# Optimization experiments

Hardware: AMD Instinct MI355X
Metric: run time of the kernel (lower is better)

## Reference

```python
import jax, jax.numpy as jnp
import numpy as np

EPS_L2 = 1e-6   # featureL2Norm epsilon
EPS_MM = 1e-5   # MutualMatching epsilon
K_POOL = 2      # relocalization_k_size


def feature_l2norm(f):
    # torch: f / sqrt(sum(f^2, dim=1) + eps)
    norm = jnp.sqrt(jnp.sum(f * f, axis=1, keepdims=True) + EPS_L2)
    return f / norm


def mutual_matching(c):
    # c: [b, 1, f1, f2, f3, f4]
    b_max = jnp.max(c, axis=(2, 3), keepdims=True)  # max over source positions
    a_max = jnp.max(c, axis=(4, 5), keepdims=True)  # max over target positions
    return c * (c / (a_max + EPS_MM)) * (c / (b_max + EPS_MM))


def maxpool4d_max(c, k):
    # c: [b, 1, H, W, H2, W2] -> strided 4D max pool (max over all k^4 offsets)
    b = c.shape[0]
    H, W, H2, W2 = c.shape[2:]
    x = c[:, 0].reshape(b, H // k, k, W // k, k, H2 // k, k, W2 // k, k)
    x = x.transpose(0, 1, 3, 5, 7, 2, 4, 6, 8)
    x = x.reshape(b, H // k, W // k, H2 // k, W2 // k, k ** 4)
    return jnp.max(x, axis=-1)[:, None]  # [b,1,H/k,W/k,H2/k,W2/k]


def conv4d(x, w, b):
    # x: [N, Cin, d1, d2, d3, d4], w: [Cout, Cin, 3,3,3,3], SAME padding (pre-pad 1)
    y = jax.lax.conv_general_dilated(x, w, window_strides=(1, 1, 1, 1), padding='SAME')
    return y + b.reshape(1, -1, 1, 1, 1, 1)


def setup_inputs() -> dict:
    key = jax.random.key(0)
    ks = jax.random.split(key, 8)
    B, C, H, W = 8, 1024, 48, 48
    return {
        'feature_A': jax.random.normal(ks[0], (B, C, H, W), dtype=jnp.float32),
        'feature_B': jax.random.normal(ks[1], (B, C, H, W), dtype=jnp.float32),
        'w1': jax.random.normal(ks[2], (10, 1, 3, 3, 3, 3), dtype=jnp.float32) * 0.05,
        'b1': jnp.zeros((10,), dtype=jnp.float32),
        'w2': jax.random.normal(ks[3], (10, 10, 3, 3, 3, 3), dtype=jnp.float32) * 0.05,
        'b2': jnp.zeros((10,), dtype=jnp.float32),
        'w3': jax.random.normal(ks[4], (1, 10, 3, 3, 3, 3), dtype=jnp.float32) * 0.05,
        'b3': jnp.zeros((1,), dtype=jnp.float32),
    }


def reference(feature_A, feature_B, w1, b1, w2, b2, w3, b3):
    # 1) L2-normalize features over channels
    fa = feature_l2norm(feature_A)
    fb = feature_l2norm(feature_B)
    b, c, h, w = fa.shape
    # 2) 4D correlation: [b, hA*wA, hB*wB]
    corr = jnp.einsum('bcp,bcq->bpq', fa.reshape(b, c, h * w), fb.reshape(b, c, h * w))
    corr = corr.reshape(b, 1, h, w, h, w)
    # ReLU + featureL2Norm over singleton channel dim => x / sqrt(x^2 + eps)
    corr = jax.nn.relu(corr)
    corr = corr / jnp.sqrt(corr * corr + EPS_L2)
    # 3) strided 4D max pool (relocalization)
    corr = maxpool4d_max(corr, K_POOL)
    # 4) mutual matching
    corr = mutual_matching(corr)
    x = jax.nn.relu(conv4d(corr, w1, b1))
    x = jax.nn.relu(conv4d(x, w2, b2))
    x = jax.nn.relu(conv4d(x, w3, b3))
    # 6) mutual matching again
    return mutual_matching(x)
```

## Files before the change

### kernel.cpp

```cpp
#include <hip/hip_runtime.h>
#include <hip/hip_bf16.h>
#include <math.h>

#define C_   1024
#define P_   2304
#define S4   331776

typedef __attribute__((ext_vector_type(8))) short short8;
typedef __attribute__((ext_vector_type(4))) float f32x4;
typedef __attribute__((ext_vector_type(4))) unsigned int u32x4;

__device__ inline unsigned short f2bf(float v) {
  unsigned u = __builtin_bit_cast(unsigned, v);
  u += 0x7fffu + ((u >> 16) & 1u);
  return (unsigned short)(u >> 16);
}
__device__ inline float bf2f(unsigned short h) {
  unsigned u = ((unsigned)h) << 16;
  return __builtin_bit_cast(float, u);
}

__device__ inline void async16(const void* g, void* l) {
  __builtin_amdgcn_global_load_lds(
      (const __attribute__((address_space(1))) unsigned int*)g,
      (__attribute__((address_space(3))) unsigned int*)l, 16, 0, 0);
}

__global__ __launch_bounds__(256) void k_prep(
    const float* __restrict__ fA, const float* __restrict__ fB,
    unsigned short* __restrict__ TAhi, unsigned short* __restrict__ TAlo,
    unsigned short* __restrict__ TBhi, unsigned short* __restrict__ TBlo,
    float* __restrict__ part) {
  __shared__ float ld[64 * 65];
  __shared__ float pslds[512];
  const int c0 = blockIdx.x * 64, p0 = blockIdx.y * 64;
  const int fb = blockIdx.z, f = fb >> 3, b = fb & 7;
  const float* src = (f ? fB : fA) + (size_t)b * C_ * P_;
  unsigned short* Thi = (f ? TBhi : TAhi) + (size_t)b * P_ * C_;
  unsigned short* Tlo = (f ? TBlo : TAlo) + (size_t)b * P_ * C_;
  const int t = threadIdx.x;
#pragma unroll
  for (int e = 0; e < 4; ++e) {
    int cid = t + e * 256;
    int r = cid >> 4, ch = cid & 15;
    float4 v = *(const float4*)&src[(size_t)(c0 + r) * P_ + p0 + ch * 4];
    ld[r * 65 + ch * 4 + 0] = v.x;
    ld[r * 65 + ch * 4 + 1] = v.y;
    ld[r * 65 + ch * 4 + 2] = v.z;
    ld[r * 65 + ch * 4 + 3] = v.w;
  }
  __syncthreads();
#pragma unroll
  for (int e = 0; e < 2; ++e) {
    int ocid = t + e * 256;
    int pl = ocid >> 3, c8 = ocid & 7;
    unsigned short hi[8], lo[8];
    float sq = 0.f;
#pragma unroll
    for (int s = 0; s < 8; ++s) {
      float v = ld[(c8 * 8 + s) * 65 + pl];
      unsigned short h = f2bf(v);
      float rem = v - bf2f(h);
      hi[s] = h; lo[s] = f2bf(rem);
      sq = fmaf(v, v, sq);
    }
    size_t go = (size_t)(p0 + pl) * C_ + c0 + c8 * 8;
    *(uint4*)&Thi[go] = *(uint4*)hi;
    *(uint4*)&Tlo[go] = *(uint4*)lo;
    pslds[ocid] = sq;
  }
  __syncthreads();
  if (t < 64) {
    float s = 0.f;
#pragma unroll
    for (int c8 = 0; c8 < 8; ++c8) s += pslds[t * 8 + c8];
    part[((size_t)fb * 16 + blockIdx.x) * P_ + p0 + t] = s;
  }
}

__global__ void k_invnorm(const float* __restrict__ part, float* __restrict__ inv) {
  int p = blockIdx.x * 256 + threadIdx.x;
  int fb = blockIdx.y;
  float s = 1e-6f;
  for (int ct = 0; ct < 16; ++ct) s += part[((size_t)fb * 16 + ct) * P_ + p];
  inv[(size_t)fb * P_ + p] = 1.0f / sqrtf(s);
}

__global__ __launch_bounds__(256, 3) void k_corr_mfma(
    const unsigned short* __restrict__ TAhi_, const unsigned short* __restrict__ TAlo_,
    const unsigned short* __restrict__ TBhi_, const unsigned short* __restrict__ TBlo_,
    const float* __restrict__ invn, float* __restrict__ pooled) {
  __shared__ __align__(16) char lds_raw[36864];
  float* epi = (float*)lds_raw;

  const int b = blockIdx.y;
  const size_t tb = (size_t)b * P_ * C_;
  const unsigned short* TAhi = TAhi_ + tb;
  const unsigned short* TAlo = TAlo_ + tb;
  const unsigned short* TBhi = TBhi_ + tb;
  const unsigned short* TBlo = TBlo_ + tb;
  float* out = pooled + (size_t)b * S4;

  const int g = blockIdx.x;
  const int xcd = g & 7, idx = g >> 3;
  const int ti = (xcd & 1) * 6 + idx % 6;
  const int tj = (xcd >> 1) * 6 + idx / 6;
  const int p0 = ti * 192, q0 = tj * 96;
  const int t = threadIdx.x;
  const int lane = t & 63, w = t >> 6;
  const int wr = w >> 1, wc = w & 1;
  const int m15 = lane & 15, q4 = lane >> 4;
  const int laneoff = (q4 ^ ((m15 >> 1) & 3)) * 16;

  f32x4 acc[6][3];
#pragma unroll
  for (int a = 0; a < 6; ++a)
#pragma unroll
    for (int c = 0; c < 3; ++c) acc[a][c] = (f32x4){0.f, 0.f, 0.f, 0.f};

  const unsigned short* gld[9];
  int ldsb[9];
#pragma unroll
  for (int e = 0; e < 9; ++e) {
    int chunk = (w * 9 + e) * 64 + lane;
    int row = chunk >> 2, cpos = chunk & 3;
    int cglob = cpos ^ ((row >> 1) & 3);
    const unsigned short* bp; int roff;
    if (row < 192)      { bp = TAhi; roff = p0 + row; }
    else if (row < 384) { bp = TAlo; roff = p0 + row - 192; }
    else if (row < 480) { bp = TBhi; roff = q0 + row - 384; }
    else                { bp = TBlo; roff = q0 + row - 480; }
    gld[e] = bp + (size_t)roff * C_ + cglob * 8;
    ldsb[e] = (w * 9 + e) * 1024;
  }

  auto STAGE = [&](int kt) {
#pragma unroll
    for (int e = 0; e < 9; ++e)
      async16(gld[e] + kt, lds_raw + ldsb[e]);
  };

  for (int kt = 0; kt < C_; kt += 32) {
    __syncthreads();
    STAGE(kt);
    asm volatile("s_waitcnt vmcnt(0)" ::: "memory");
    __syncthreads();

    const char* buf = lds_raw;
    short8 bh[3], bl[3];
#pragma unroll
    for (int c = 0; c < 3; ++c) {
      int rB = (384 + wc * 48 + c * 16 + m15) * 64;
      bh[c] = *(const short8*)(buf + rB + laneoff);
      bl[c] = *(const short8*)(buf + rB + 6144 + laneoff);
    }
#pragma unroll
    for (int a = 0; a < 6; ++a) {
      int rA = (wr * 96 + a * 16 + m15) * 64;
      short8 ah = *(const short8*)(buf + rA + laneoff);
      short8 al = *(const short8*)(buf + rA + 12288 + laneoff);
#pragma unroll
      for (int c = 0; c < 3; ++c)
        acc[a][c] = __builtin_amdgcn_mfma_f32_16x16x32_bf16(ah, bh[c], acc[a][c], 0, 0, 0);
#pragma unroll
      for (int c = 0; c < 3; ++c)
        acc[a][c] = __builtin_amdgcn_mfma_f32_16x16x32_bf16(ah, bl[c], acc[a][c], 0, 0, 0);
#pragma unroll
      for (int c = 0; c < 3; ++c)
        acc[a][c] = __builtin_amdgcn_mfma_f32_16x16x32_bf16(al, bh[c], acc[a][c], 0, 0, 0);
    }
  }
  __syncthreads();

  const float* invA = invn + (size_t)b * P_;
  const float* invB = invn + (size_t)(8 + b) * P_;
  float ibv[3];
#pragma unroll
  for (int c = 0; c < 3; ++c) ibv[c] = invB[q0 + wc * 48 + c * 16 + m15];
#pragma unroll
  for (int a = 0; a < 6; ++a) {
    float4 ia = *(const float4*)&invA[p0 + wr * 96 + a * 16 + q4 * 4];
    int h_local = wr * 2 + (a >= 3 ? 1 : 0);
    int wbase = (a % 3) * 8 + q4 * 2;
#pragma unroll
    for (int c = 0; c < 3; ++c) {
      float v0 = acc[a][c][0] * ia.x * ibv[c];
      float v1 = acc[a][c][1] * ia.y * ibv[c];
      float v2 = acc[a][c][2] * ia.z * ibv[c];
      float v3 = acc[a][c][3] * ia.w * ibv[c];
      float m0 = fmaxf(v0, v1), m1 = fmaxf(v2, v3);
      m0 = fmaxf(m0, __shfl_xor(m0, 1, 64));
      m1 = fmaxf(m1, __shfl_xor(m1, 1, 64));
      if (!(m15 & 1)) {
        int ql2 = wc * 24 + c * 8 + (m15 >> 1);
        epi[(h_local * 24 + wbase + 0) * 50 + ql2] = m0;
        epi[(h_local * 24 + wbase + 1) * 50 + ql2] = m1;
      }
    }
  }
  __syncthreads();

  for (int ix = t; ix < 1152; ix += 256) {
    int orow = ix / 24, ocol = ix % 24;
    int dlt = orow / 24, wp = orow % 24;
    const float* r0 = &epi[((dlt * 2 + 0) * 24 + wp) * 50];
    const float* r1 = &epi[((dlt * 2 + 1) * 24 + wp) * 50];
    float m = fmaxf(fmaxf(r0[ocol], r0[24 + ocol]),
                    fmaxf(r1[ocol], r1[24 + ocol]));
    float r = fmaxf(m, 0.f);
    float v = r / sqrtf(r * r + 1e-6f);
    out[(size_t)(ti * 48 + orow) * 576 + tj * 24 + ocol] = v;
  }
}

__global__ void k_rowmax(const float* __restrict__ x, float* __restrict__ amax) {
  int row = blockIdx.x;
  const float* r = x + (size_t)row * 576;
  float m = -1e30f;
  for (int e = threadIdx.x; e < 576; e += 64) m = fmaxf(m, r[e]);
  for (int off = 32; off > 0; off >>= 1) m = fmaxf(m, __shfl_down(m, off, 64));
  if (threadIdx.x == 0) amax[row] = m;
}

__global__ void k_colmax(const float* __restrict__ x, float* __restrict__ bmax) {
  __shared__ float pl[4][64];
  int b = blockIdx.x, klc = blockIdx.y * 64;
  int t = threadIdx.x;
  int kl = klc + (t & 63), seg = t >> 6;
  const float* xb = x + (size_t)b * S4;
  float m = -1e30f;
  for (int ij = seg * 144; ij < (seg + 1) * 144; ++ij)
    m = fmaxf(m, xb[(size_t)ij * 576 + kl]);
  pl[seg][t & 63] = m;
  __syncthreads();
  if (t < 64) {
    float r = fmaxf(fmaxf(pl[0][t], pl[1][t]), fmaxf(pl[2][t], pl[3][t]));
    bmax[b * 576 + klc + t] = r;
  }
}

__global__ void k_mm_apply(const float* __restrict__ x,
                           const float* __restrict__ amax,
                           const float* __restrict__ bmax,
                           float* __restrict__ y) {
  int i = blockIdx.x * 256 + threadIdx.x;
  int b = i / S4, r = i % S4;
  int ij = r / 576, kl = r % 576;
  float c = x[i];
  y[i] = c * (c / (amax[b * 576 + ij] + 1e-5f)) * (c / (bmax[b * 576 + kl] + 1e-5f));
}

__global__ __launch_bounds__(192, 4) void k_conv1_pack(
    const float* __restrict__ x, const float* __restrict__ w,
    const float* __restrict__ bias, unsigned int* __restrict__ C1p) {
  __shared__ float tile[9 * 702];
  const float* xb = x + (size_t)S4 * blockIdx.y;
  unsigned int* yb = C1p + ((size_t)blockIdx.y * 576 + blockIdx.x) * 6912;
  const int ij = blockIdx.x;
  const int i = ij / 24, j = ij % 24;
  const int t = threadIdx.x;
  const int k = t >> 3;
  const int l0 = (t & 7) * 3;

  if (t < 152) yb[6760 + t] = 0u;
  if (t < 100) {
    int kk, ll;
    if (t < 26)      { kk = 0;          ll = t; }
    else if (t < 52) { kk = 25;         ll = t - 26; }
    else if (t < 76) { kk = t - 52 + 1; ll = 0; }
    else             { kk = t - 76 + 1; ll = 25; }
    unsigned int* p = yb + (kk * 26 + ll) * 10;
#pragma unroll
    for (int q = 0; q < 10; ++q) p[q] = 0u;
  }

  int soff[4]; bool eok[4], klok[4]; int eidx[4];
#pragma unroll
  for (int q = 0; q < 4; ++q) {
    int e = t + q * 192;
    eidx[q] = e; eok[q] = (e < 702);
    int row = e / 27, col = e % 27;
    klok[q] = (row >= 1 && row < 25 && col >= 1 && col < 25);
    soff[q] = (row - 1) * 24 + (col - 1);
  }

  float acc[10][3];
#pragma unroll
  for (int co = 0; co < 10; ++co)
#pragma unroll
    for (int oo = 0; oo < 3; ++oo) acc[co][oo] = 0.f;

#pragma unroll
  for (int pln = 0; pln < 9; ++pln) {
    int ii = i + pln / 3 - 1, jj = j + pln % 3 - 1;
    const bool slab_ok = (ii >= 0 && ii < 24 && jj >= 0 && jj < 24);
    const float* src = xb + (size_t)(ii * 24 + jj) * 576;
#pragma unroll
    for (int q = 0; q < 4; ++q) {
      if (eok[q]) {
        float v = 0.f;
        if (slab_ok && klok[q]) v = src[soff[q]];
        tile[pln * 702 + eidx[q]] = v;
      }
    }
  }
  __syncthreads();
#pragma unroll
  for (int pln = 0; pln < 9; ++pln) {
    const float* base = &tile[pln * 702 + k * 27 + l0];
#pragma unroll
    for (int dk = 0; dk < 3; ++dk) {
      float c0 = base[dk * 27 + 0], c1 = base[dk * 27 + 1],
            c2 = base[dk * 27 + 2], c3 = base[dk * 27 + 3],
            c4 = base[dk * 27 + 4];
#pragma unroll
      for (int co = 0; co < 10; ++co) {
        const float* wr = w + (size_t)co * 81 + pln * 9 + dk * 3;
        float w0 = wr[0], w1 = wr[1], w2v = wr[2];
        acc[co][0] = fmaf(w0, c0, acc[co][0]);
        acc[co][0] = fmaf(w1, c1, acc[co][0]);
        acc[co][0] = fmaf(w2v, c2, acc[co][0]);
        acc[co][1] = fmaf(w0, c1, acc[co][1]);
        acc[co][1] = fmaf(w1, c2, acc[co][1]);
        acc[co][1] = fmaf(w2v, c3, acc[co][1]);
        acc[co][2] = fmaf(w0, c2, acc[co][2]);
        acc[co][2] = fmaf(w1, c3, acc[co][2]);
        acc[co][2] = fmaf(w2v, c4, acc[co][2]);
      }
    }
  }
#pragma unroll
  for (int oo = 0; oo < 3; ++oo) {
    unsigned int* baseo = yb + ((k + 1) * 26 + (l0 + oo + 1)) * 10;
#pragma unroll
    for (int co = 0; co < 10; ++co) {
      float v = fmaxf(acc[co][oo] + bias[co], 0.f);
      unsigned short hi = f2bf(v);
      unsigned short lo = f2bf(v - bf2f(hi));
      baseo[co] = ((unsigned)hi << 16) | (unsigned)lo;
    }
  }
}

__global__ void k_packw2(const float* __restrict__ w2,
                         unsigned short* __restrict__ P1,
                         unsigned short* __restrict__ P2) {
  int idx = blockIdx.x * 256 + threadIdx.x;
  if (idx >= 30720) return;
  int tap = idx >> 10;
  int h   = (idx >> 9) & 1;
  int n   = (idx >> 5) & 15;
  int kp  = idx & 31;
  int k   = h * 16 + (kp >> 1);
  float v = 0.f;
  if (tap < 27 && n < 10 && k < 30) {
    int ci = k % 10, dl = k / 10;
    v = w2[(size_t)(n * 10 + ci) * 81 + tap * 3 + dl];
  }
  unsigned short hi = f2bf(v);
  unsigned short lo = f2bf(v - bf2f(hi));
  P1[idx] = hi;
  P2[idx] = (kp & 1) ? lo : (unsigned short)0;
}

__global__ void k_packw3(const float* __restrict__ w3,
                         unsigned short* __restrict__ Bh,
                         unsigned short* __restrict__ Bl) {
  int idx = blockIdx.x * 256 + threadIdx.x;
  if (idx >= 4608) return;
  int s = idx >> 9;
  int n = (idx >> 5) & 15;
  int kap = idx & 31;
  float v = 0.f;
  if (n < 3 && kap < 30) {
    int ci = kap % 10, dl = kap / 10;
    v = w3[(size_t)ci * 81 + s * 9 + n * 3 + dl];
  }
  unsigned short hi = f2bf(v);
  unsigned short lo = f2bf(v - bf2f(hi));
  Bh[idx] = hi; Bl[idx] = lo;
}

__global__ __launch_bounds__(256, 2) void k_conv2_mfma(
    const unsigned int* __restrict__ C1p,
    const unsigned short* __restrict__ Wp1, const unsigned short* __restrict__ Wp2,
    const float* __restrict__ bias, unsigned int* __restrict__ C2p) {
  __shared__ __align__(16) unsigned int lds[2 * 7168];
  const int b = blockIdx.y, ij = blockIdx.x;
  const int i = ij / 24, j = ij % 24;
  const int t = threadIdx.x, lane = t & 63, w = t >> 6;
  const int m15 = lane & 15, q4 = lane >> 4;

  unsigned int* yb = C2p + ((size_t)b * 576 + ij) * 6912;
  if (t < 152) yb[6760 + t] = 0u;
  if (t < 100) {
    int kk, ll;
    if (t < 26)      { kk = 0;          ll = t; }
    else if (t < 52) { kk = 25;         ll = t - 26; }
    else if (t < 76) { kk = t - 52 + 1; ll = 0; }
    else             { kk = t - 76 + 1; ll = 25; }
    unsigned int* p = yb + (kk * 26 + ll) * 10;
#pragma unroll
    for (int q = 0; q < 10; ++q) p[q] = 0u;
  }

  int rowb[9];
#pragma unroll
  for (int mi = 0; mi < 9; ++mi) {
    int kl = (w * 9 + mi) * 16 + m15;
    int kk = kl / 24, ll = kl % 24;
    rowb[mi] = ((kk + 1) * 26 + ll) * 10;
  }

  const unsigned int* sptr[9]; int tb[9];
#pragma unroll
  for (int s = 0; s < 9; ++s) {
    int di = s / 3 - 1, dj = s % 3 - 1;
    int ii = i + di, jj = j + dj;
    bool v = ((unsigned)ii < 24u) && ((unsigned)jj < 24u);
    sptr[s] = C1p + ((size_t)b * 576 + (size_t)(v ? (ii * 24 + jj) : ij)) * 6912;
    tb[s] = v ? s * 3 : 27;
  }

  auto STAGE = [&](const unsigned int* sp, int par) {
#pragma unroll
    for (int r = 0; r < 7; ++r) {
      const int g = w * 7 + r;
      const unsigned int* gp = sp + (g < 27 ? g * 256 : 0) + lane * 4;
      async16(gp, (char*)lds + par * 28672 + g * 1024);
    }
  };

  f32x4 acc[9];
#pragma unroll
  for (int mi = 0; mi < 9; ++mi) acc[mi] = (f32x4){0.f, 0.f, 0.f, 0.f};

  STAGE(sptr[0], 0);

#pragma unroll
  for (int s = 0; s < 9; ++s) {
    const int par = s & 1;
    short8 p1[3][2], p2[3][2];
#pragma unroll
    for (int dk = 0; dk < 3; ++dk)
#pragma unroll
      for (int h = 0; h < 2; ++h) {
        size_t o = (size_t)(((tb[s] + dk) * 2 + h) * 16 + m15) * 32 + (size_t)q4 * 8;
        p1[dk][h] = *(const short8*)(Wp1 + o);
        p2[dk][h] = *(const short8*)(Wp2 + o);
      }
    if (s < 8) {
      STAGE(sptr[s + 1], par ^ 1);
      asm volatile("s_waitcnt vmcnt(7)" ::: "memory");
    } else {
      asm volatile("s_waitcnt vmcnt(0)" ::: "memory");
    }
    __builtin_amdgcn_s_barrier();
    __builtin_amdgcn_sched_barrier(0);

    const unsigned int* buf = lds + par * 7168;
#pragma unroll
    for (int dk = 0; dk < 3; ++dk) {
#pragma unroll
      for (int mi = 0; mi < 9; ++mi) {
        const char* base = (const char*)(buf + (rowb[mi] + (dk - 1) * 260)) + q4 * 16;
        uint2 a00 = *(const uint2*)(base);
        uint2 a01 = *(const uint2*)(base + 8);
        uint2 a10 = *(const uint2*)(base + 64);
        uint2 a11 = *(const uint2*)(base + 72);
        short8 a0 = __builtin_bit_cast(short8, (u32x4){a00.x, a00.y, a01.x, a01.y});
        short8 a1 = __builtin_bit_cast(short8, (u32x4){a10.x, a10.y, a11.x, a11.y});
        acc[mi] = __builtin_amdgcn_mfma_f32_16x16x32_bf16(a0, p1[dk][0], acc[mi], 0, 0, 0);
        acc[mi] = __builtin_amdgcn_mfma_f32_16x16x32_bf16(a0, p2[dk][0], acc[mi], 0, 0, 0);
        acc[mi] = __builtin_amdgcn_mfma_f32_16x16x32_bf16(a1, p1[dk][1], acc[mi], 0, 0, 0);
        acc[mi] = __builtin_amdgcn_mfma_f32_16x16x32_bf16(a1, p2[dk][1], acc[mi], 0, 0, 0);
      }
    }
    __builtin_amdgcn_sched_barrier(0);
    __builtin_amdgcn_s_barrier();
  }

  if (m15 < 10) {
    const float bv = bias[m15];
#pragma unroll
    for (int mi = 0; mi < 9; ++mi) {
#pragma unroll
      for (int reg = 0; reg < 4; ++reg) {
        int kl = (w * 9 + mi) * 16 + q4 * 4 + reg;
        int kk = kl / 24 + 1, ll = kl % 24 + 1;
        float v = fmaxf(acc[mi][reg] + bv, 0.f);
        unsigned short hi = f2bf(v);
        unsigned short lo = f2bf(v - bf2f(hi));
        yb[(kk * 26 + ll) * 10 + m15] = ((unsigned)hi << 16) | (unsigned)lo;
      }
    }
  }
}

__global__ __launch_bounds__(256, 2) void k_conv3_mfma(
    const unsigned int* __restrict__ C2p,
    const unsigned short* __restrict__ Bh, const unsigned short* __restrict__ Bl,
    const float* __restrict__ bias, float* __restrict__ C3) {
  __shared__ __align__(16) unsigned int lds[2 * 7168];
  const int b = blockIdx.y, ij = blockIdx.x;
  const int i = ij / 24, j = ij % 24;
  const int t = threadIdx.x, lane = t & 63, w = t >> 6;
  const int m15 = lane & 15, q4 = lane >> 4;

  int rowb[10];
#pragma unroll
  for (int mi = 0; mi < 10; ++mi) {
    int m = (w * 10 + mi) * 16 + m15;
    int kp = m / 24, l = m % 24;
    rowb[mi] = (m < 624) ? (kp * 26 + l) * 10 : 0;
  }

  bool sval[9];
  const unsigned int* sptr[9];
#pragma unroll
  for (int s = 0; s < 9; ++s) {
    int di = s / 3 - 1, dj = s % 3 - 1;
    int ii = i + di, jj = j + dj;
    bool v = ((unsigned)ii < 24u) && ((unsigned)jj < 24u);
    sval[s] = v;
    sptr[s] = C2p + ((size_t)b * 576 + (size_t)(v ? (ii * 24 + jj) : ij)) * 6912;
  }

  short8 BHk[9], BLk[9];
#pragma unroll
  for (int s = 0; s < 9; ++s) {
    size_t o = (size_t)(s * 16 + m15) * 32 + (size_t)q4 * 8;
    BHk[s] = *(const short8*)(Bh + o);
    BLk[s] = *(const short8*)(Bl + o);
  }

  auto STAGE = [&](const unsigned int* sp, int par) {
#pragma unroll
    for (int r = 0; r < 7; ++r) {
      const int g = w * 7 + r;
      const unsigned int* gp = sp + (g < 27 ? g * 256 : 0) + lane * 4;
      async16(gp, (char*)lds + par * 28672 + g * 1024);
    }
  };

  f32x4 acc[10];
#pragma unroll
  for (int mi = 0; mi < 10; ++mi) acc[mi] = (f32x4){0.f, 0.f, 0.f, 0.f};

  STAGE(sptr[0], 0);

#pragma unroll
  for (int s = 0; s < 9; ++s) {
    const int par = s & 1;
    if (s < 8) {
      STAGE(sptr[s + 1], par ^ 1);
      asm volatile("s_waitcnt vmcnt(7)" ::: "memory");
    } else {
      asm volatile("s_waitcnt vmcnt(0)" ::: "memory");
    }
    __builtin_amdgcn_s_barrier();
    __builtin_amdgcn_sched_barrier(0);
    if (sval[s]) {
      const unsigned int* buf = lds + par * 7168;
#pragma unroll
      for (int mi = 0; mi < 10; ++mi) {
        const uint2* p = (const uint2*)(buf + rowb[mi] + q4 * 8);
        uint2 d0 = p[0], d1 = p[1], d2 = p[2], d3 = p[3];
        u32x4 hd, lv;
        hd.x = __builtin_amdgcn_perm(d0.y, d0.x, 0x07060302u);
        hd.y = __builtin_amdgcn_perm(d1.y, d1.x, 0x07060302u);
        hd.z = __builtin_amdgcn_perm(d2.y, d2.x, 0x07060302u);
        hd.w = __builtin_amdgcn_perm(d3.y, d3.x, 0x07060302u);
        lv.x = __builtin_amdgcn_perm(d0.y, d0.x, 0x05040100u);
        lv.y = __builtin_amdgcn_perm(d1.y, d1.x, 0x05040100u);
        lv.z = __builtin_amdgcn_perm(d2.y, d2.x, 0x05040100u);
        lv.w = __builtin_amdgcn_perm(d3.y, d3.x, 0x05040100u);
        short8 ah = __builtin_bit_cast(short8, hd);
        short8 al = __builtin_bit_cast(short8, lv);
        acc[mi] = __builtin_amdgcn_mfma_f32_16x16x32_bf16(ah, BHk[s], acc[mi], 0, 0, 0);
        acc[mi] = __builtin_amdgcn_mfma_f32_16x16x32_bf16(ah, BLk[s], acc[mi], 0, 0, 0);
        acc[mi] = __builtin_amdgcn_mfma_f32_16x16x32_bf16(al, BHk[s], acc[mi], 0, 0, 0);
      }
    }
    __builtin_amdgcn_sched_barrier(0);
    __builtin_amdgcn_s_barrier();
  }

  float* u = (float*)lds;
  if (m15 < 3) {
#pragma unroll
    for (int mi = 0; mi < 10; ++mi)
#pragma unroll
      for (int reg = 0; reg < 4; ++reg) {
        int m = (w * 10 + mi) * 16 + q4 * 4 + reg;
        u[m * 4 + m15] = acc[mi][reg];
      }
  }
  __syncthreads();
  const float bv = bias[0];
  float* outp = C3 + (size_t)b * S4 + (size_t)ij * 576;
  for (int idx = t; idx < 576; idx += 256) {
    int k = idx / 24, l = idx % 24;
    float sum = u[((k + 0) * 24 + l) * 4 + 0]
              + u[((k + 1) * 24 + l) * 4 + 1]
              + u[((k + 2) * 24 + l) * 4 + 2];
    outp[idx] = fmaxf(sum + bv, 0.f);
  }
}

extern "C" void kernel_launch(void* const* d_in, const int* in_sizes, int n_in,
                              void* d_out, int out_size, void* d_ws, size_t ws_size,
                              hipStream_t stream) {
  const float* fA = (const float*)d_in[0];
  const float* fB = (const float*)d_in[1];
  const float* w1 = (const float*)d_in[2];
  const float* b1 = (const float*)d_in[3];
  const float* w2 = (const float*)d_in[4];
  const float* b2 = (const float*)d_in[5];
  const float* w3 = (const float*)d_in[6];
  const float* b3 = (const float*)d_in[7];
  float* out = (float*)d_out;
  float* ws = (float*)d_ws;
  (void)in_sizes; (void)n_in; (void)out_size; (void)ws_size;

  unsigned int* C1p  = (unsigned int*)ws;
  unsigned int* C2p  = (unsigned int*)(ws + 31850496);
  unsigned short* TAhi = (unsigned short*)ws;
  unsigned short* TAlo = TAhi + (size_t)8 * P_ * C_;
  unsigned short* TBhi = TAlo + (size_t)8 * P_ * C_;
  unsigned short* TBlo = TBhi + (size_t)8 * P_ * C_;
  float* pooled = ws + 37748736;
  float* part   = ws + 40402944;
  float* invn   = ws + 40992768;
  float* amax1  = ws + 41029632;
  float* bmax1  = ws + 41034240;
  float* C3     = ws + 0;
  float* amax2  = ws + 2654208;
  float* bmax2  = ws + 2658816;
  unsigned short* Bh3 = (unsigned short*)(ws + 63700992);
  unsigned short* Bl3 = Bh3 + 4608;
  unsigned short* Wp2a = (unsigned short*)d_out;
  unsigned short* Wp2b = Wp2a + 30720;

  k_prep<<<dim3(16, 36, 16), 256, 0, stream>>>(fA, fB, TAhi, TAlo, TBhi, TBlo, part);
  k_invnorm<<<dim3(9, 16), 256, 0, stream>>>(part, invn);
  k_corr_mfma<<<dim3(288, 8), 256, 0, stream>>>(TAhi, TAlo, TBhi, TBlo, invn, pooled);

  k_rowmax<<<dim3(8 * 576), 64, 0, stream>>>(pooled, amax1);
  k_colmax<<<dim3(8, 9), 256, 0, stream>>>(pooled, bmax1);
  k_mm_apply<<<dim3(10368), 256, 0, stream>>>(pooled, amax1, bmax1, pooled);

  k_packw2<<<dim3(120), 256, 0, stream>>>(w2, Wp2a, Wp2b);
  k_packw3<<<dim3(18), 256, 0, stream>>>(w3, Bh3, Bl3);
  k_conv1_pack<<<dim3(576, 8), 192, 0, stream>>>(pooled, w1, b1, C1p);
  k_conv2_mfma<<<dim3(576, 8), 256, 0, stream>>>(C1p, Wp2a, Wp2b, b2, C2p);
  k_conv3_mfma<<<dim3(576, 8), 256, 0, stream>>>(C2p, Bh3, Bl3, b3, C3);

  k_rowmax<<<dim3(8 * 576), 64, 0, stream>>>(C3, amax2);
  k_colmax<<<dim3(8, 9), 256, 0, stream>>>(C3, bmax2);
  k_mm_apply<<<dim3(10368), 256, 0, stream>>>(C3, amax2, bmax2, out);
}
```

Before: 1.018 ms.

## Restructure conv2 MFMA to put dk taps in N dim and reduce in LDS

The conv2 kernel now folds the third spatial tap (dk) into the MFMA N dimension (5 output channels × 3 dk per group, two groups) instead of looping over dk with shifted A rows. A loads drop from 3 per source slice to 1, and the 16-wide N tile is filled with 15 useful columns instead of 10. The partial results are written to LDS and a shifted sum over dk is done in an epilogue. Invalid neighbour slices are now skipped instead of multiplied by zero weights, and the block index is swizzled for locality. The cost is 20 accumulators per wave instead of 9, and an extra LDS reduction pass with syncs.

```diff
diff --git a/kernel.cpp b/kernel.cpp
--- a/kernel.cpp
+++ b/kernel.cpp
@@ -346,16 +346,19 @@
                          unsigned short* __restrict__ P1,
                          unsigned short* __restrict__ P2) {
   int idx = blockIdx.x * 256 + threadIdx.x;
-  if (idx >= 30720) return;
-  int tap = idx >> 10;
-  int h   = (idx >> 9) & 1;
-  int n   = (idx >> 5) & 15;
-  int kp  = idx & 31;
-  int k   = h * 16 + (kp >> 1);
+  if (idx >= 18432) return;
+  int s  = idx >> 11;
+  int g  = (idx >> 10) & 1;
+  int h  = (idx >> 9) & 1;
+  int n  = (idx >> 5) & 15;
+  int kp = idx & 31;
+  int k  = h * 16 + (kp >> 1);
   float v = 0.f;
-  if (tap < 27 && n < 10 && k < 30) {
+  if (n < 15 && k < 30) {
+    int cop = n / 3, dk = n % 3;
+    int co = g * 5 + cop;
     int ci = k % 10, dl = k / 10;
-    v = w2[(size_t)(n * 10 + ci) * 81 + tap * 3 + dl];
+    v = w2[(size_t)(co * 10 + ci) * 81 + s * 9 + dk * 3 + dl];
   }
   unsigned short hi = f2bf(v);
   unsigned short lo = f2bf(v - bf2f(hi));
@@ -386,7 +389,9 @@
     const unsigned short* __restrict__ Wp1, const unsigned short* __restrict__ Wp2,
     const float* __restrict__ bias, unsigned int* __restrict__ C2p) {
   __shared__ __align__(16) unsigned int lds[2 * 7168];
-  const int b = blockIdx.y, ij = blockIdx.x;
+  const int b = blockIdx.y;
+  const int x = blockIdx.x;
+  const int ij = (x & 7) * 72 + (x >> 3);
   const int i = ij / 24, j = ij % 24;
   const int t = threadIdx.x, lane = t & 63, w = t >> 6;
   const int m15 = lane & 15, q4 = lane >> 4;
@@ -404,22 +409,23 @@
     for (int q = 0; q < 10; ++q) p[q] = 0u;
   }
 
-  int rowb[9];
-#pragma unroll
-  for (int mi = 0; mi < 9; ++mi) {
-    int kl = (w * 9 + mi) * 16 + m15;
-    int kk = kl / 24, ll = kl % 24;
-    rowb[mi] = ((kk + 1) * 26 + ll) * 10;
-  }
-
-  const unsigned int* sptr[9]; int tb[9];
+  int rowb[10];
+#pragma unroll
+  for (int mi = 0; mi < 10; ++mi) {
+    int m = (w * 10 + mi) * 16 + m15;
+    int kp = m / 24, l = m % 24;
+    rowb[mi] = (m < 624) ? (kp * 26 + l) * 10 : 0;
+  }
+
+  bool sval[9];
+  const unsigned int* sptr[9];
 #pragma unroll
   for (int s = 0; s < 9; ++s) {
     int di = s / 3 - 1, dj = s % 3 - 1;
     int ii = i + di, jj = j + dj;
     bool v = ((unsigned)ii < 24u) && ((unsigned)jj < 24u);
+    sval[s] = v;
     sptr[s] = C1p + ((size_t)b * 576 + (size_t)(v ? (ii * 24 + jj) : ij)) * 6912;
-    tb[s] = v ? s * 3 : 27;
   }
 
   auto STAGE = [&](const unsigned int* sp, int par) {
@@ -431,23 +437,25 @@
     }
   };
 
-  f32x4 acc[9];
-#pragma unroll
-  for (int mi = 0; mi < 9; ++mi) acc[mi] = (f32x4){0.f, 0.f, 0.f, 0.f};
+  f32x4 acc[10][2];
+#pragma unroll
+  for (int mi = 0; mi < 10; ++mi)
+#pragma unroll
+    for (int g = 0; g < 2; ++g) acc[mi][g] = (f32x4){0.f, 0.f, 0.f, 0.f};
 
   STAGE(sptr[0], 0);
 
 #pragma unroll
   for (int s = 0; s < 9; ++s) {
     const int par = s & 1;
-    short8 p1[3][2], p2[3][2];
-#pragma unroll
-    for (int dk = 0; dk < 3; ++dk)
+    short8 p1[2][2], p2[2][2];
+#pragma unroll
+    for (int g = 0; g < 2; ++g)
 #pragma unroll
       for (int h = 0; h < 2; ++h) {
-        size_t o = (size_t)(((tb[s] + dk) * 2 + h) * 16 + m15) * 32 + (size_t)q4 * 8;
-        p1[dk][h] = *(const short8*)(Wp1 + o);
-        p2[dk][h] = *(const short8*)(Wp2 + o);
+        size_t o = (size_t)((((s * 2 + g) * 2 + h) * 16) + m15) * 32 + (size_t)q4 * 8;
+        p1[g][h] = *(const short8*)(Wp1 + o);
+        p2[g][h] = *(const short8*)(Wp2 + o);
       }
     if (s < 8) {
       STAGE(sptr[s + 1], par ^ 1);
@@ -458,41 +466,57 @@
     __builtin_amdgcn_s_barrier();
     __builtin_amdgcn_sched_barrier(0);
 
-    const unsigned int* buf = lds + par * 7168;
-#pragma unroll
-    for (int dk = 0; dk < 3; ++dk) {
-#pragma unroll
-      for (int mi = 0; mi < 9; ++mi) {
-        const char* base = (const char*)(buf + (rowb[mi] + (dk - 1) * 260)) + q4 * 16;
+    if (sval[s]) {
+      const unsigned int* buf = lds + par * 7168;
+#pragma unroll
+      for (int mi = 0; mi < 10; ++mi) {
+        const char* base = (const char*)(buf + rowb[mi]) + q4 * 16;
         uint2 a00 = *(const uint2*)(base);
         uint2 a01 = *(const uint2*)(base + 8);
         uint2 a10 = *(const uint2*)(base + 64);
         uint2 a11 = *(const uint2*)(base + 72);
         short8 a0 = __builtin_bit_cast(short8, (u32x4){a00.x, a00.y, a01.x, a01.y});
         short8 a1 = __builtin_bit_cast(short8, (u32x4){a10.x, a10.y, a11.x, a11.y});
-        acc[mi] = __builtin_amdgcn_mfma_f32_16x16x32_bf16(a0, p1[dk][0], acc[mi], 0, 0, 0);
-        acc[mi] = __builtin_amdgcn_mfma_f32_16x16x32_bf16(a0, p2[dk][0], acc[mi], 0, 0, 0);
-        acc[mi] = __builtin_amdgcn_mfma_f32_16x16x32_bf16(a1, p1[dk][1], acc[mi], 0, 0, 0);
-        acc[mi] = __builtin_amdgcn_mfma_f32_16x16x32_bf16(a1, p2[dk][1], acc[mi], 0, 0, 0);
+#pragma unroll
+        for (int g = 0; g < 2; ++g) {
+          acc[mi][g] = __builtin_amdgcn_mfma_f32_16x16x32_bf16(a0, p1[g][0], acc[mi][g], 0, 0, 0);
+          acc[mi][g] = __builtin_amdgcn_mfma_f32_16x16x32_bf16(a0, p2[g][0], acc[mi][g], 0, 0, 0);
+          acc[mi][g] = __builtin_amdgcn_mfma_f32_16x16x32_bf16(a1, p1[g][1], acc[mi][g], 0, 0, 0);
+          acc[mi][g] = __builtin_amdgcn_mfma_f32_16x16x32_bf16(a1, p2[g][1], acc[mi][g], 0, 0, 0);
+        }
       }
     }
     __builtin_amdgcn_sched_barrier(0);
     __builtin_amdgcn_s_barrier();
   }
 
-  if (m15 < 10) {
-    const float bv = bias[m15];
-#pragma unroll
-    for (int mi = 0; mi < 9; ++mi) {
-#pragma unroll
-      for (int reg = 0; reg < 4; ++reg) {
-        int kl = (w * 9 + mi) * 16 + q4 * 4 + reg;
-        int kk = kl / 24 + 1, ll = kl % 24 + 1;
-        float v = fmaxf(acc[mi][reg] + bv, 0.f);
-        unsigned short hi = f2bf(v);
-        unsigned short lo = f2bf(v - bf2f(hi));
-        yb[(kk * 26 + ll) * 10 + m15] = ((unsigned)hi << 16) | (unsigned)lo;
-      }
+  float* u = (float*)lds;
+#pragma unroll
+  for (int g = 0; g < 2; ++g) {
+    __syncthreads();
+    if (m15 < 15) {
+#pragma unroll
+      for (int mi = 0; mi < 10; ++mi)
+#pragma unroll
+        for (int reg = 0; reg < 4; ++reg) {
+          int m = (w * 10 + mi) * 16 + q4 * 4 + reg;
+          u[m * 15 + m15] = acc[mi][g][reg];
+        }
+    }
+    __syncthreads();
+    for (int idx = t; idx < 2880; idx += 256) {
+      int cop = idx / 576;
+      int co = g * 5 + cop;
+      int r = idx % 576;
+      int k = r / 24, l = r % 24;
+      float s = bias[co];
+#pragma unroll
+      for (int dk = 0; dk < 3; ++dk)
+        s += u[((k + dk) * 24 + l) * 15 + cop * 3 + dk];
+      float v = fmaxf(s, 0.f);
+      unsigned short hi = f2bf(v);
+      unsigned short lo = f2bf(v - bf2f(hi));
+      yb[((k + 1) * 26 + (l + 1)) * 10 + co] = ((unsigned)hi << 16) | (unsigned)lo;
     }
   }
 }
@@ -640,7 +664,7 @@
   unsigned short* Bh3 = (unsigned short*)(ws + 63700992);
   unsigned short* Bl3 = Bh3 + 4608;
   unsigned short* Wp2a = (unsigned short*)d_out;
-  unsigned short* Wp2b = Wp2a + 30720;
+  unsigned short* Wp2b = Wp2a + 18432;
 
   k_prep<<<dim3(16, 36, 16), 256, 0, stream>>>(fA, fB, TAhi, TAlo, TBhi, TBlo, part);
   k_invnorm<<<dim3(9, 16), 256, 0, stream>>>(part, invn);
@@ -650,7 +674,7 @@
   k_colmax<<<dim3(8, 9), 256, 0, stream>>>(pooled, bmax1);
   k_mm_apply<<<dim3(10368), 256, 0, stream>>>(pooled, amax1, bmax1, pooled);
 
-  k_packw2<<<dim3(120), 256, 0, stream>>>(w2, Wp2a, Wp2b);
+  k_packw2<<<dim3(72), 256, 0, stream>>>(w2, Wp2a, Wp2b);
   k_packw3<<<dim3(18), 256, 0, stream>>>(w3, Bh3, Bl3);
   k_conv1_pack<<<dim3(576, 8), 192, 0, stream>>>(pooled, w1, b1, C1p);
   k_conv2_mfma<<<dim3(576, 8), 256, 0, stream>>>(C1p, Wp2a, Wp2b, b2, C2p);
```

After: 983.6 us. 3.4% less time.
